# Kernel optimization log

Hardware: AMD Instinct MI355X
Metric: run time of the kernel (lower is better)

## Reference

```python
import jax, jax.numpy as jnp
import numpy as np

C = 256
GROUPS = 8
EPS_GN = 1e-5
EPS_ATTN = 1e-6


def setup_inputs() -> dict:
    key = jax.random.key(0)
    ks = jax.random.split(key, 10)
    b, c, h, w = 8, C, 128, 128
    # xavier_uniform for 1x1 conv weight [out, in]: limit = sqrt(6/(in+out))
    lim = float(np.sqrt(6.0 / (c + c)))
    mkw = lambda k: jax.random.uniform(k, (c, c), jnp.float32, -lim, lim)
    return {
        "x": jax.random.normal(ks[0], (b, c, h, w), jnp.float32),
        "gamma": jnp.ones((c,), jnp.float32),
        "beta": jnp.zeros((c,), jnp.float32),
        "Wq": mkw(ks[1]), "bq": jnp.zeros((c,), jnp.float32),
        "Wk": mkw(ks[2]), "bk": jnp.zeros((c,), jnp.float32),
        "Wv": mkw(ks[3]), "bv": jnp.zeros((c,), jnp.float32),
        "Wp": mkw(ks[4]), "bp": jnp.zeros((c,), jnp.float32),
    }


def _group_norm(x, gamma, beta):
    b, c, h, w = x.shape
    xg = x.reshape(b, GROUPS, c // GROUPS, h, w)
    mean = xg.mean(axis=(2, 3, 4), keepdims=True)
    var = xg.var(axis=(2, 3, 4), keepdims=True)
    xn = ((xg - mean) * jax.lax.rsqrt(var + EPS_GN)).reshape(b, c, h, w)
    return xn * gamma[None, :, None, None] + beta[None, :, None, None]


def _conv1x1(x, W, bias):
    # 1x1 conv == per-pixel matmul: [b,c,h,w] x [o,c] -> [b,o,h,w]
    return jnp.einsum('bchw,oc->bohw', x, W) + bias[None, :, None, None]


def reference(x, gamma, beta, Wq, bq, Wk, bk, Wv, bv, Wp, bp):
    b, c, h, w = x.shape
    xn = _group_norm(x, gamma, beta)
    q = jax.nn.elu(_conv1x1(xn, Wq, bq)) + 1.0
    k = jax.nn.elu(_conv1x1(xn, Wk, bk)) + 1.0
    v = _conv1x1(xn, Wv, bv)
    n = h * w
    q = q.reshape(b, c, n)
    k = k.reshape(b, c, n)
    v = v.reshape(b, c, n)
    kv = jnp.einsum('bcn,bdn->bcd', k, v)          # k @ v^T, [b,c,c]
    k_sum = jnp.sum(k, axis=2, keepdims=True)       # [b,c,1]
    kv = kv / (k_sum + EPS_ATTN)
    out = jnp.einsum('bcd,bdn->bcn', kv, q).reshape(b, c, h, w)
    out = _conv1x1(out, Wp, bp)
    return out + x
```

## Files before the change

### kernel.cpp

```cpp
#include <hip/hip_runtime.h>

typedef unsigned short u16;
using bf16x8 = __attribute__((ext_vector_type(8))) __bf16;
using f32x4  = __attribute__((ext_vector_type(4))) float;

#define BATCH 8
#define CH    256
#define NPIX  16384
#define GN_EPS   1e-5f
#define ATTN_EPS 1e-6f

__device__ __forceinline__ u16 f2bf(float f) {
  unsigned int u = __float_as_uint(f);
  u += 0x7fffu + ((u >> 16) & 1u);
  return (u16)(u >> 16);
}

__global__ void stats_kernel(const float* __restrict__ x, float* __restrict__ sum,
                             float* __restrict__ sqs) {
  const int gi = blockIdx.x >> 3;
  const int sp = blockIdx.x & 7;
  const float4* p = (const float4*)x + (size_t)gi * 131072 + (size_t)sp * 16384;
  float s = 0.f, ss = 0.f;
  for (int i = 0; i < 64; ++i) {
    float4 v = p[threadIdx.x + i * 256];
    s  += v.x + v.y + v.z + v.w;
    ss += v.x * v.x + v.y * v.y + v.z * v.z + v.w * v.w;
  }
  for (int off = 32; off; off >>= 1) {
    s  += __shfl_xor(s, off);
    ss += __shfl_xor(ss, off);
  }
  __shared__ float rs[4], rss[4];
  const int wave = threadIdx.x >> 6, lane = threadIdx.x & 63;
  if (!lane) { rs[wave] = s; rss[wave] = ss; }
  __syncthreads();
  if (!threadIdx.x) {
    atomicAdd(&sum[gi], rs[0] + rs[1] + rs[2] + rs[3]);
    atomicAdd(&sqs[gi], rss[0] + rss[1] + rss[2] + rss[3]);
  }
}

__global__ void finalize_kernel(const float* __restrict__ sums, const float* __restrict__ sqs,
                                const float* __restrict__ gamma, const float* __restrict__ beta,
                                float* __restrict__ sA, float* __restrict__ sB) {
  const int t = blockIdx.x * 256 + threadIdx.x;
  const int c = t & 255;
  const int gi = (t >> 8) * 8 + (c >> 5);
  const float inv = 1.f / 524288.f;
  const float mean = sums[gi] * inv;
  const float var = sqs[gi] * inv - mean * mean;
  const float rstd = rsqrtf(var + GN_EPS);
  const float a = rstd * gamma[c];
  sA[t] = a;
  sB[t] = beta[c] - mean * a;
}

__global__ __launch_bounds__(256) void foldw_kernel(
    const float* __restrict__ Wq, const float* __restrict__ bq,
    const float* __restrict__ Wk, const float* __restrict__ bk,
    const float* __restrict__ sA, const float* __restrict__ sB,
    u16* __restrict__ Wqb, u16* __restrict__ Wkb,
    float* __restrict__ bqf, float* __restrict__ bkf) {
  const int b = blockIdx.x >> 4;
  const int rt = blockIdx.x & 15;
  const int tid = threadIdx.x;
  const int wave = tid >> 6, lane = tid & 63;
  const float a = sA[b * 256 + tid];
  const float s = sB[b * 256 + tid];
  __shared__ float rq[4], rk[4];
  for (int i = 0; i < 16; ++i) {
    const int row = rt * 16 + i;
    const float wq = Wq[row * 256 + tid];
    const float wk = Wk[row * 256 + tid];
    Wqb[b * 65536 + row * 256 + tid] = f2bf(wq * a);
    Wkb[b * 65536 + row * 256 + tid] = f2bf(wk * a);
    float pq = wq * s, pk = wk * s;
    for (int off = 32; off; off >>= 1) {
      pq += __shfl_xor(pq, off);
      pk += __shfl_xor(pk, off);
    }
    if (!lane) { rq[wave] = pq; rk[wave] = pk; }
    __syncthreads();
    if (!tid) {
      bqf[b * 256 + row] = bq[row] + rq[0] + rq[1] + rq[2] + rq[3];
      bkf[b * 256 + row] = bk[row] + rk[0] + rk[1] + rk[2] + rk[3];
    }
    __syncthreads();
  }
}

__global__ __launch_bounds__(256) void wvt_kernel(const float* __restrict__ Wv,
                                                  float* __restrict__ Wvt) {
  __shared__ float t[16][17];
  const int ti = blockIdx.x & 15, tj = blockIdx.x >> 4;
  const int tx = threadIdx.x & 15, ty = threadIdx.x >> 4;
  t[ty][tx] = Wv[(tj * 16 + ty) * 256 + ti * 16 + tx];
  __syncthreads();
  Wvt[(ti * 16 + ty) * 256 + tj * 16 + tx] = t[tx][ty];
}

__global__ __launch_bounds__(1024, 4) void fused_t_kernel(
    const float* __restrict__ x, const u16* __restrict__ Wkb, const float* __restrict__ bkf,
    float* __restrict__ ksum, float* __restrict__ tdst, int mode) {
  __shared__ __align__(16) u16 xnv[64 * 288];
  __shared__ __align__(16) u16 xcm[256 * 72];
  __shared__ __align__(16) u16 Kcp[256 * 72];

  const int b  = blockIdx.x & 7;
  const int sp = blockIdx.x >> 3;
  const int tid = threadIdx.x;
  const int wave = tid >> 6;
  const int lane = tid & 63;
  const int m = lane & 15;
  const int q = lane >> 4;

  const int ctg = wave & 7;
  const int ptg = wave >> 3;
  const int ckg = wave >> 2;
  const int cvg = wave & 3;

  const float* xb = x + (size_t)b * CH * NPIX;
  const u16* Wkbb = Wkb + b * 65536;

  float biasv[2][4];
#pragma unroll
  for (int i = 0; i < 2; ++i)
#pragma unroll
    for (int r = 0; r < 4; ++r)
      biasv[i][r] = bkf[b * 256 + (2 * ctg + i) * 16 + q * 4 + r];

  f32x4 accT[4][4];
#pragma unroll
  for (int i = 0; i < 4; ++i)
#pragma unroll
    for (int j = 0; j < 4; ++j) accT[i][j] = {0.f, 0.f, 0.f, 0.f};
  float ksum_acc = 0.f;

  const int p_ = tid & 63;
  const int cq = tid >> 6;

  for (int ch = 0; ch < 8; ++ch) {
    const int pix0 = sp * 512 + ch * 64;
    __syncthreads();
#pragma unroll
    for (int i = 0; i < 4; ++i) {
      const int c = (cq + 16 * i) * 4;
      const float v0 = __builtin_nontemporal_load(&xb[(size_t)(c + 0) * NPIX + pix0 + p_]);
      const float v1 = __builtin_nontemporal_load(&xb[(size_t)(c + 1) * NPIX + pix0 + p_]);
      const float v2 = __builtin_nontemporal_load(&xb[(size_t)(c + 2) * NPIX + pix0 + p_]);
      const float v3 = __builtin_nontemporal_load(&xb[(size_t)(c + 3) * NPIX + pix0 + p_]);
      const u16 b0 = f2bf(v0), b1 = f2bf(v1), b2 = f2bf(v2), b3 = f2bf(v3);
      const unsigned int lo = (unsigned int)b0 | ((unsigned int)b1 << 16);
      const unsigned int hi = (unsigned int)b2 | ((unsigned int)b3 << 16);
      *(uint2*)&xnv[p_ * 288 + (c ^ ((p_ & 7) << 3))] = make_uint2(lo, hi);
      xcm[(c + 0) * 72 + p_] = b0;
      xcm[(c + 1) * 72 + p_] = b1;
      xcm[(c + 2) * 72 + p_] = b2;
      xcm[(c + 3) * 72 + p_] = b3;
    }
    __syncthreads();

    f32x4 ac[2][2];
#pragma unroll
    for (int i = 0; i < 2; ++i)
#pragma unroll
      for (int pp = 0; pp < 2; ++pp) ac[i][pp] = {0.f, 0.f, 0.f, 0.f};
#pragma unroll
    for (int ks = 0; ks < 8; ++ks) {
      const bf16x8 a0 = *(const bf16x8*)(Wkbb + ((2 * ctg + 0) * 16 + m) * 256 + ks * 32 + q * 8);
      const bf16x8 a1 = *(const bf16x8*)(Wkbb + ((2 * ctg + 1) * 16 + m) * 256 + ks * 32 + q * 8);
#pragma unroll
      for (int pp = 0; pp < 2; ++pp) {
        const int prow = (2 * ptg + pp) * 16 + m;
        const bf16x8 bfr =
            *(const bf16x8*)&xnv[prow * 288 + ((ks * 32 + q * 8) ^ ((prow & 7) << 3))];
        ac[0][pp] = __builtin_amdgcn_mfma_f32_16x16x32_bf16(a0, bfr, ac[0][pp], 0, 0, 0);
        ac[1][pp] = __builtin_amdgcn_mfma_f32_16x16x32_bf16(a1, bfr, ac[1][pp], 0, 0, 0);
      }
    }
#pragma unroll
    for (int i = 0; i < 2; ++i) {
#pragma unroll
      for (int r = 0; r < 4; ++r) {
        const int row = (2 * ctg + i) * 16 + q * 4 + r;
        const float bias = biasv[i][r];
#pragma unroll
        for (int pp = 0; pp < 2; ++pp) {
          float v = ac[i][pp][r] + bias;
          v = v > 0.f ? v + 1.f : __expf(v);
          Kcp[row * 72 + (2 * ptg + pp) * 16 + m] = f2bf(v);
        }
      }
    }
    __syncthreads();

    {
      const int krow = tid & 255;
      const int kseg = tid >> 8;
      const bf16x8 k0 = *(const bf16x8*)&Kcp[krow * 72 + kseg * 16];
      const bf16x8 k1 = *(const bf16x8*)&Kcp[krow * 72 + kseg * 16 + 8];
      float s = 0.f;
#pragma unroll
      for (int j = 0; j < 8; ++j) s += (float)k0[j] + (float)k1[j];
      ksum_acc += s;
    }

#pragma unroll
    for (int ks = 0; ks < 2; ++ks) {
      bf16x8 af[4], bfv[4];
#pragma unroll
      for (int i = 0; i < 4; ++i)
        af[i] = *(const bf16x8*)&Kcp[((4 * ckg + i) * 16 + m) * 72 + ks * 32 + q * 8];
#pragma unroll
      for (int j = 0; j < 4; ++j)
        bfv[j] = *(const bf16x8*)&xcm[((4 * cvg + j) * 16 + m) * 72 + ks * 32 + q * 8];
#pragma unroll
      for (int i = 0; i < 4; ++i)
#pragma unroll
        for (int j = 0; j < 4; ++j)
          accT[i][j] = __builtin_amdgcn_mfma_f32_16x16x32_bf16(af[i], bfv[j], accT[i][j], 0, 0, 0);
    }
  }

  atomicAdd(&ksum[b * CH + (tid & 255)], ksum_acc);
  if (mode == 0) {
    float* Tp = tdst + (size_t)blockIdx.x * 65536 + wave * 4096 + lane * 4;
#pragma unroll
    for (int i = 0; i < 4; ++i)
#pragma unroll
      for (int j = 0; j < 4; ++j)
        __builtin_nontemporal_store(accT[i][j], (f32x4*)(Tp + (i * 4 + j) * 256));
  } else {
    float* Tb2 = tdst + (size_t)b * 65536;
#pragma unroll
    for (int i = 0; i < 4; ++i)
#pragma unroll
      for (int j = 0; j < 4; ++j)
#pragma unroll
        for (int r = 0; r < 4; ++r) {
          const int row = (4 * ckg + i) * 16 + q * 4 + r;
          const int col = (4 * cvg + j) * 16 + m;
          atomicAdd(&Tb2[row * CH + col], accT[i][j][r]);
        }
  }
}

__global__ __launch_bounds__(256) void treduce_kernel(const float* __restrict__ part,
                                                      float* __restrict__ Traw) {
  const int b = blockIdx.x >> 4;
  const int w = blockIdx.x & 15;
  __shared__ float tile[64][65];
  const size_t base = (size_t)w * 4096;
  for (int k = 0; k < 16; ++k) {
    const int o = k * 256 + threadIdx.x;
    float s = 0.f;
#pragma unroll 8
    for (int sp = 0; sp < 32; ++sp)
      s += __builtin_nontemporal_load(&part[(size_t)(sp * 8 + b) * 65536 + base + o]);
    const int lanef = (o >> 2) & 63;
    const int r = o & 3;
    const int e4 = o >> 8;
    const int i = e4 >> 2, j = e4 & 3;
    const int mm = lanef & 15, qq = lanef >> 4;
    tile[i * 16 + qq * 4 + r][j * 16 + mm] = s;
  }
  __syncthreads();
  const int ckg = w >> 2, cvg = w & 3;
  float* dst = Traw + (size_t)b * 65536 + (size_t)(ckg * 64) * 256 + cvg * 64;
  const int col = threadIdx.x & 63;
  const int r0 = threadIdx.x >> 6;
#pragma unroll
  for (int k = 0; k < 16; ++k) {
    const int lr = r0 * 16 + k;
    dst[(size_t)lr * 256 + col] = tile[lr][col];
  }
}

__global__ __launch_bounds__(256) void m1_kernel(
    const float* __restrict__ Wp, const float* __restrict__ Traw,
    const float* __restrict__ ksum, const float* __restrict__ sA,
    const float* __restrict__ sB, float* __restrict__ A1, float* __restrict__ s1) {
  __shared__ float WpLT[256 * 16];
  __shared__ float ksL[256];
  const int b = blockIdx.x >> 4;
  const int rt = blockIdx.x & 15;
  const int tid = threadIdx.x;
  const float kk = ksum[b * 256 + tid];
  ksL[tid] = kk;
  const float rs = 1.f / (kk + ATTN_EPS);
#pragma unroll
  for (int r = 0; r < 16; ++r)
    WpLT[tid * 16 + r] = Wp[(rt * 16 + r) * 256 + tid] * rs;
  __syncthreads();
  float acc[16], s1a[16];
#pragma unroll
  for (int r = 0; r < 16; ++r) { acc[r] = 0.f; s1a[r] = 0.f; }
  const float* Tb = Traw + (size_t)b * 65536;
  for (int k = 0; k < 256; ++k) {
    const float v = Tb[k * 256 + tid];
    const float kv = ksL[k];
#pragma unroll
    for (int r4 = 0; r4 < 4; ++r4) {
      const f32x4 w4 = *(const f32x4*)&WpLT[k * 16 + r4 * 4];
#pragma unroll
      for (int e = 0; e < 4; ++e) {
        acc[r4 * 4 + e] += w4[e] * v;
        s1a[r4 * 4 + e] += w4[e] * kv;
      }
    }
  }
  const float av = sA[b * 256 + tid], sv = sB[b * 256 + tid];
#pragma unroll
  for (int r = 0; r < 16; ++r)
    A1[(size_t)b * 65536 + (rt * 16 + r) * 256 + tid] = av * acc[r] + sv * s1a[r];
  if (tid == 0) {
#pragma unroll
    for (int r = 0; r < 16; ++r) s1[b * 256 + rt * 16 + r] = s1a[r];
  }
}

__global__ __launch_bounds__(256) void m2_kernel(
    const float* __restrict__ A1, const float* __restrict__ Wvt,
    const float* __restrict__ bv, const float* __restrict__ s1,
    u16* __restrict__ Mb) {
  __shared__ float ALT[256 * 16];
  const int b = blockIdx.x >> 4;
  const int rt = blockIdx.x & 15;
  const int tid = threadIdx.x;
#pragma unroll
  for (int r = 0; r < 16; ++r)
    ALT[tid * 16 + r] = A1[(size_t)b * 65536 + (rt * 16 + r) * 256 + tid];
  __syncthreads();
  float acc[16];
#pragma unroll
  for (int r = 0; r < 16; ++r) acc[r] = 0.f;
  for (int ci = 0; ci < 256; ++ci) {
    const float wv = Wvt[ci * 256 + tid];
#pragma unroll
    for (int r4 = 0; r4 < 4; ++r4) {
      const f32x4 a4 = *(const f32x4*)&ALT[ci * 16 + r4 * 4];
#pragma unroll
      for (int e = 0; e < 4; ++e) acc[r4 * 4 + e] += a4[e] * wv;
    }
  }
  const float bvd = bv[tid];
#pragma unroll
  for (int r = 0; r < 16; ++r)
    Mb[(size_t)b * 65536 + (rt * 16 + r) * 256 + tid] =
        f2bf(acc[r] + bvd * s1[b * 256 + rt * 16 + r]);
}

__global__ __launch_bounds__(256, 4) void out_kernel(
    const float* __restrict__ x, const u16* __restrict__ Wqb, const float* __restrict__ bqf,
    const u16* __restrict__ Mb, const float* __restrict__ bp, float* __restrict__ out) {
  __shared__ __align__(16) u16 buf[64 * 288];
  const int b = blockIdx.x & 7;
  const int pix0 = (blockIdx.x >> 3) * 64;
  const int tid = threadIdx.x;
  const int wave = tid >> 6;
  const int lane = tid & 63;
  const int m = lane & 15;
  const int q = lane >> 4;

  const float* xb = x + (size_t)b * CH * NPIX;
  const u16* Wqbb = Wqb + b * 65536;

  const int p_ = tid & 63;
  const int cq = tid >> 6;
#pragma unroll
  for (int i = 0; i < 16; ++i) {
    const int c = (cq + 4 * i) * 4;
    const float v0 = __builtin_nontemporal_load(&xb[(size_t)(c + 0) * NPIX + pix0 + p_]);
    const float v1 = __builtin_nontemporal_load(&xb[(size_t)(c + 1) * NPIX + pix0 + p_]);
    const float v2 = __builtin_nontemporal_load(&xb[(size_t)(c + 2) * NPIX + pix0 + p_]);
    const float v3 = __builtin_nontemporal_load(&xb[(size_t)(c + 3) * NPIX + pix0 + p_]);
    const unsigned int lo = (unsigned int)f2bf(v0) | ((unsigned int)f2bf(v1) << 16);
    const unsigned int hi = (unsigned int)f2bf(v2) | ((unsigned int)f2bf(v3) << 16);
    *(uint2*)&buf[p_ * 288 + (c ^ ((p_ & 7) << 3))] = make_uint2(lo, hi);
  }
  __syncthreads();

  f32x4 aq[4][4];
#pragma unroll
  for (int pt = 0; pt < 4; ++pt)
#pragma unroll
    for (int ct = 0; ct < 4; ++ct) aq[pt][ct] = {0.f, 0.f, 0.f, 0.f};
#pragma unroll
  for (int ks = 0; ks < 8; ++ks) {
    bf16x8 af[4];
#pragma unroll
    for (int pt = 0; pt < 4; ++pt) {
      const int prow = pt * 16 + m;
      af[pt] = *(const bf16x8*)&buf[prow * 288 + ((ks * 32 + q * 8) ^ ((prow & 7) << 3))];
    }
#pragma unroll
    for (int ct = 0; ct < 4; ++ct) {
      const bf16x8 bfr = *(const bf16x8*)(Wqbb + ((4 * wave + ct) * 16 + m) * 256 + ks * 32 + q * 8);
#pragma unroll
      for (int pt = 0; pt < 4; ++pt)
        aq[pt][ct] = __builtin_amdgcn_mfma_f32_16x16x32_bf16(af[pt], bfr, aq[pt][ct], 0, 0, 0);
    }
  }
  __syncthreads();
#pragma unroll
  for (int ct = 0; ct < 4; ++ct) {
    const int c2 = (4 * wave + ct) * 16 + m;
    const float bias = bqf[b * 256 + c2];
#pragma unroll
    for (int pt = 0; pt < 4; ++pt)
#pragma unroll
      for (int r = 0; r < 4; ++r) {
        float v = aq[pt][ct][r] + bias;
        v = v > 0.f ? v + 1.f : __expf(v);
        const int prow = pt * 16 + q * 4 + r;
        buf[prow * 288 + (c2 ^ ((prow & 7) << 3))] = f2bf(v);
      }
  }
  __syncthreads();

  f32x4 ao[4][4];
#pragma unroll
  for (int ct = 0; ct < 4; ++ct)
#pragma unroll
    for (int pt = 0; pt < 4; ++pt) ao[ct][pt] = {0.f, 0.f, 0.f, 0.f};
  const u16* Ab = Mb + (size_t)b * 65536;
#pragma unroll
  for (int ks = 0; ks < 8; ++ks) {
    bf16x8 af2[4];
#pragma unroll
    for (int ct = 0; ct < 4; ++ct)
      af2[ct] = *(const bf16x8*)(Ab + ((4 * wave + ct) * 16 + m) * 256 + ks * 32 + q * 8);
#pragma unroll
    for (int pt = 0; pt < 4; ++pt) {
      const int brow = pt * 16 + m;
      const bf16x8 bfr = *(const bf16x8*)&buf[brow * 288 + ((ks * 32 + q * 8) ^ ((brow & 7) << 3))];
#pragma unroll
      for (int ct = 0; ct < 4; ++ct)
        ao[ct][pt] = __builtin_amdgcn_mfma_f32_16x16x32_bf16(af2[ct], bfr, ao[ct][pt], 0, 0, 0);
    }
  }
  float* ob = out + (size_t)b * CH * NPIX;
#pragma unroll
  for (int ct = 0; ct < 4; ++ct)
#pragma unroll
    for (int r = 0; r < 4; ++r) {
      const int row = (4 * wave + ct) * 16 + q * 4 + r;
      const float bias = bp[row];
#pragma unroll
      for (int pt = 0; pt < 4; ++pt) {
        const int idx = row * NPIX + pix0 + pt * 16 + m;
        const float xr = __builtin_nontemporal_load(&xb[idx]);
        __builtin_nontemporal_store(ao[ct][pt][r] + bias + xr, &ob[idx]);
      }
    }
}

extern "C" void kernel_launch(void* const* d_in, const int* in_sizes, int n_in,
                              void* d_out, int out_size, void* d_ws, size_t ws_size,
                              hipStream_t stream) {
  const float* x     = (const float*)d_in[0];
  const float* gamma = (const float*)d_in[1];
  const float* beta  = (const float*)d_in[2];
  const float* Wq    = (const float*)d_in[3];
  const float* bq    = (const float*)d_in[4];
  const float* Wk    = (const float*)d_in[5];
  const float* bk    = (const float*)d_in[6];
  const float* Wv    = (const float*)d_in[7];
  const float* bv    = (const float*)d_in[8];
  const float* Wp    = (const float*)d_in[9];
  const float* bp    = (const float*)d_in[10];
  float* out = (float*)d_out;

  float* wsf  = (float*)d_ws;
  float* sum  = wsf;
  float* sqs  = wsf + 64;
  float* ksum = wsf + 128;
  float* sA   = wsf + 2176;
  float* sB   = wsf + 4224;
  float* s1   = wsf + 6272;
  float* bkf  = wsf + 8320;
  float* bqf  = wsf + 10368;
  float* Wvt  = wsf + 12416;
  float* Traw = wsf + 77952;
  float* A1   = wsf + 602240;
  u16* Wqb = (u16*)(wsf + 1126528);
  u16* Wkb = Wqb + 524288;
  u16* Mb  = (u16*)(wsf + 1650816);

  const bool bigws = ws_size >= ((size_t)72 << 20);
  float* Tpart = bigws ? (wsf + ((size_t)1 << 21)) : Traw;
  const int mode = bigws ? 0 : 1;

  hipMemsetAsync(wsf, 0, (size_t)(bigws ? 2176 : 602240) * sizeof(float), stream);
  stats_kernel<<<512, 256, 0, stream>>>(x, sum, sqs);
  finalize_kernel<<<8, 256, 0, stream>>>(sum, sqs, gamma, beta, sA, sB);
  wvt_kernel<<<256, 256, 0, stream>>>(Wv, Wvt);
  foldw_kernel<<<128, 256, 0, stream>>>(Wq, bq, Wk, bk, sA, sB, Wqb, Wkb, bqf, bkf);
  fused_t_kernel<<<256, 1024, 0, stream>>>(x, Wkb, bkf, ksum, Tpart, mode);
  if (bigws) treduce_kernel<<<128, 256, 0, stream>>>(Tpart, Traw);
  m1_kernel<<<128, 256, 0, stream>>>(Wp, Traw, ksum, sA, sB, A1, s1);
  m2_kernel<<<128, 256, 0, stream>>>(A1, Wvt, bv, s1, Mb);
  out_kernel<<<2048, 256, 0, stream>>>(x, Wqb, bqf, Mb, bp, out);
}
```

Baseline: 680.6 us.

## Hold weight fragments in registers and make out/fused kernels persistent over pixel chunks

```diff
diff --git a/kernel.cpp b/kernel.cpp
--- a/kernel.cpp
+++ b/kernel.cpp
@@ -100,7 +100,7 @@
   Wvt[(ti * 16 + ty) * 256 + tj * 16 + tx] = t[tx][ty];
 }
 
-__global__ __launch_bounds__(1024, 4) void fused_t_kernel(
+__global__ __launch_bounds__(512, 2) void fused_t_kernel(
     const float* __restrict__ x, const u16* __restrict__ Wkb, const float* __restrict__ bkf,
     float* __restrict__ ksum, float* __restrict__ tdst, int mode) {
   __shared__ __align__(16) u16 xnv[64 * 288];
@@ -115,24 +115,29 @@
   const int m = lane & 15;
   const int q = lane >> 4;
 
-  const int ctg = wave & 7;
-  const int ptg = wave >> 3;
   const int ckg = wave >> 2;
   const int cvg = wave & 3;
 
   const float* xb = x + (size_t)b * CH * NPIX;
   const u16* Wkbb = Wkb + b * 65536;
 
+  bf16x8 wA[2][8];
+#pragma unroll
+  for (int i = 0; i < 2; ++i)
+#pragma unroll
+    for (int ks = 0; ks < 8; ++ks)
+      wA[i][ks] = *(const bf16x8*)(Wkbb + ((2 * wave + i) * 16 + m) * 256 + ks * 32 + q * 8);
+
   float biasv[2][4];
 #pragma unroll
   for (int i = 0; i < 2; ++i)
 #pragma unroll
     for (int r = 0; r < 4; ++r)
-      biasv[i][r] = bkf[b * 256 + (2 * ctg + i) * 16 + q * 4 + r];
-
-  f32x4 accT[4][4];
-#pragma unroll
-  for (int i = 0; i < 4; ++i)
+      biasv[i][r] = bkf[b * 256 + (2 * wave + i) * 16 + q * 4 + r];
+
+  f32x4 accT[8][4];
+#pragma unroll
+  for (int i = 0; i < 8; ++i)
 #pragma unroll
     for (int j = 0; j < 4; ++j) accT[i][j] = {0.f, 0.f, 0.f, 0.f};
   float ksum_acc = 0.f;
@@ -144,8 +149,8 @@
     const int pix0 = sp * 512 + ch * 64;
     __syncthreads();
 #pragma unroll
-    for (int i = 0; i < 4; ++i) {
-      const int c = (cq + 16 * i) * 4;
+    for (int i = 0; i < 8; ++i) {
+      const int c = (cq + 8 * i) * 4;
       const float v0 = __builtin_nontemporal_load(&xb[(size_t)(c + 0) * NPIX + pix0 + p_]);
       const float v1 = __builtin_nontemporal_load(&xb[(size_t)(c + 1) * NPIX + pix0 + p_]);
       const float v2 = __builtin_nontemporal_load(&xb[(size_t)(c + 2) * NPIX + pix0 + p_]);
@@ -161,35 +166,35 @@
     }
     __syncthreads();
 
-    f32x4 ac[2][2];
-#pragma unroll
-    for (int i = 0; i < 2; ++i)
-#pragma unroll
-      for (int pp = 0; pp < 2; ++pp) ac[i][pp] = {0.f, 0.f, 0.f, 0.f};
-#pragma unroll
-    for (int ks = 0; ks < 8; ++ks) {
-      const bf16x8 a0 = *(const bf16x8*)(Wkbb + ((2 * ctg + 0) * 16 + m) * 256 + ks * 32 + q * 8);
-      const bf16x8 a1 = *(const bf16x8*)(Wkbb + ((2 * ctg + 1) * 16 + m) * 256 + ks * 32 + q * 8);
-#pragma unroll
-      for (int pp = 0; pp < 2; ++pp) {
-        const int prow = (2 * ptg + pp) * 16 + m;
-        const bf16x8 bfr =
-            *(const bf16x8*)&xnv[prow * 288 + ((ks * 32 + q * 8) ^ ((prow & 7) << 3))];
-        ac[0][pp] = __builtin_amdgcn_mfma_f32_16x16x32_bf16(a0, bfr, ac[0][pp], 0, 0, 0);
-        ac[1][pp] = __builtin_amdgcn_mfma_f32_16x16x32_bf16(a1, bfr, ac[1][pp], 0, 0, 0);
-      }
-    }
-#pragma unroll
-    for (int i = 0; i < 2; ++i) {
-#pragma unroll
-      for (int r = 0; r < 4; ++r) {
-        const int row = (2 * ctg + i) * 16 + q * 4 + r;
-        const float bias = biasv[i][r];
+#pragma unroll
+    for (int ph = 0; ph < 2; ++ph) {
+      f32x4 ac[2][2];
+#pragma unroll
+      for (int i = 0; i < 2; ++i)
+#pragma unroll
+        for (int pp = 0; pp < 2; ++pp) ac[i][pp] = {0.f, 0.f, 0.f, 0.f};
+#pragma unroll
+      for (int ks = 0; ks < 8; ++ks) {
 #pragma unroll
         for (int pp = 0; pp < 2; ++pp) {
-          float v = ac[i][pp][r] + bias;
-          v = v > 0.f ? v + 1.f : __expf(v);
-          Kcp[row * 72 + (2 * ptg + pp) * 16 + m] = f2bf(v);
+          const int prow = (2 * ph + pp) * 16 + m;
+          const bf16x8 bfr =
+              *(const bf16x8*)&xnv[prow * 288 + ((ks * 32 + q * 8) ^ ((prow & 7) << 3))];
+          ac[0][pp] = __builtin_amdgcn_mfma_f32_16x16x32_bf16(wA[0][ks], bfr, ac[0][pp], 0, 0, 0);
+          ac[1][pp] = __builtin_amdgcn_mfma_f32_16x16x32_bf16(wA[1][ks], bfr, ac[1][pp], 0, 0, 0);
+        }
+      }
+#pragma unroll
+      for (int i = 0; i < 2; ++i) {
+#pragma unroll
+        for (int r = 0; r < 4; ++r) {
+          const int row = (2 * wave + i) * 16 + q * 4 + r;
+#pragma unroll
+          for (int pp = 0; pp < 2; ++pp) {
+            float v = ac[i][pp][r] + biasv[i][r];
+            v = v > 0.f ? v + 1.f : __expf(v);
+            Kcp[row * 72 + (2 * ph + pp) * 16 + m] = f2bf(v);
+          }
         }
       }
     }
@@ -198,49 +203,50 @@
     {
       const int krow = tid & 255;
       const int kseg = tid >> 8;
-      const bf16x8 k0 = *(const bf16x8*)&Kcp[krow * 72 + kseg * 16];
-      const bf16x8 k1 = *(const bf16x8*)&Kcp[krow * 72 + kseg * 16 + 8];
       float s = 0.f;
 #pragma unroll
-      for (int j = 0; j < 8; ++j) s += (float)k0[j] + (float)k1[j];
+      for (int t2 = 0; t2 < 4; ++t2) {
+        const bf16x8 k0 = *(const bf16x8*)&Kcp[krow * 72 + kseg * 32 + t2 * 8];
+#pragma unroll
+        for (int j = 0; j < 8; ++j) s += (float)k0[j];
+      }
       ksum_acc += s;
     }
 
 #pragma unroll
     for (int ks = 0; ks < 2; ++ks) {
-      bf16x8 af[4], bfv[4];
-#pragma unroll
-      for (int i = 0; i < 4; ++i)
-        af[i] = *(const bf16x8*)&Kcp[((4 * ckg + i) * 16 + m) * 72 + ks * 32 + q * 8];
+      bf16x8 bfv[4];
 #pragma unroll
       for (int j = 0; j < 4; ++j)
         bfv[j] = *(const bf16x8*)&xcm[((4 * cvg + j) * 16 + m) * 72 + ks * 32 + q * 8];
 #pragma unroll
-      for (int i = 0; i < 4; ++i)
+      for (int i = 0; i < 8; ++i) {
+        const bf16x8 afi = *(const bf16x8*)&Kcp[((8 * ckg + i) * 16 + m) * 72 + ks * 32 + q * 8];
 #pragma unroll
         for (int j = 0; j < 4; ++j)
-          accT[i][j] = __builtin_amdgcn_mfma_f32_16x16x32_bf16(af[i], bfv[j], accT[i][j], 0, 0, 0);
+          accT[i][j] = __builtin_amdgcn_mfma_f32_16x16x32_bf16(afi, bfv[j], accT[i][j], 0, 0, 0);
+      }
     }
   }
 
   atomicAdd(&ksum[b * CH + (tid & 255)], ksum_acc);
   if (mode == 0) {
-    float* Tp = tdst + (size_t)blockIdx.x * 65536 + wave * 4096 + lane * 4;
-#pragma unroll
-    for (int i = 0; i < 4; ++i)
+    float* Tp = tdst + (size_t)blockIdx.x * 65536 + wave * 8192 + lane * 4;
+#pragma unroll
+    for (int i = 0; i < 8; ++i)
 #pragma unroll
       for (int j = 0; j < 4; ++j)
-        __builtin_nontemporal_store(accT[i][j], (f32x4*)(Tp + (i * 4 + j) * 256));
+        *(f32x4*)(Tp + (i * 4 + j) * 256) = accT[i][j];
   } else {
     float* Tb2 = tdst + (size_t)b * 65536;
 #pragma unroll
-    for (int i = 0; i < 4; ++i)
+    for (int i = 0; i < 8; ++i)
 #pragma unroll
       for (int j = 0; j < 4; ++j)
 #pragma unroll
         for (int r = 0; r < 4; ++r) {
-          const int row = (4 * ckg + i) * 16 + q * 4 + r;
-          const int col = (4 * cvg + j) * 16 + m;
+          const int row = ckg * 128 + i * 16 + q * 4 + r;
+          const int col = cvg * 64 + j * 16 + m;
           atomicAdd(&Tb2[row * CH + col], accT[i][j][r]);
         }
   }
@@ -248,32 +254,35 @@
 
 __global__ __launch_bounds__(256) void treduce_kernel(const float* __restrict__ part,
                                                       float* __restrict__ Traw) {
-  const int b = blockIdx.x >> 4;
-  const int w = blockIdx.x & 15;
-  __shared__ float tile[64][65];
-  const size_t base = (size_t)w * 4096;
-  for (int k = 0; k < 16; ++k) {
-    const int o = k * 256 + threadIdx.x;
-    float s = 0.f;
+  const int b = blockIdx.x >> 5;
+  const int w = (blockIdx.x >> 2) & 7;
+  const int s = blockIdx.x & 3;
+  const int tid = threadIdx.x;
+  __shared__ float tile[32][65];
+  const int base = w * 8192 + s * 2048;
+  for (int k = 0; k < 8; ++k) {
+    const int f = base + k * 256 + tid;
+    float acc = 0.f;
 #pragma unroll 8
-    for (int sp = 0; sp < 32; ++sp)
-      s += __builtin_nontemporal_load(&part[(size_t)(sp * 8 + b) * 65536 + base + o]);
-    const int lanef = (o >> 2) & 63;
-    const int r = o & 3;
-    const int e4 = o >> 8;
-    const int i = e4 >> 2, j = e4 & 3;
+    for (int spp = 0; spp < 32; ++spp)
+      acc += part[(size_t)(spp * 8 + b) * 65536 + f];
+    const int il = k >> 2;
+    const int j = k & 3;
+    const int lanef = tid >> 2;
+    const int r = tid & 3;
     const int mm = lanef & 15, qq = lanef >> 4;
-    tile[i * 16 + qq * 4 + r][j * 16 + mm] = s;
+    tile[il * 16 + qq * 4 + r][j * 16 + mm] = acc;
   }
   __syncthreads();
-  const int ckg = w >> 2, cvg = w & 3;
-  float* dst = Traw + (size_t)b * 65536 + (size_t)(ckg * 64) * 256 + cvg * 64;
-  const int col = threadIdx.x & 63;
-  const int r0 = threadIdx.x >> 6;
-#pragma unroll
-  for (int k = 0; k < 16; ++k) {
-    const int lr = r0 * 16 + k;
-    dst[(size_t)lr * 256 + col] = tile[lr][col];
+  const int rowbase = (w >> 2) * 128 + s * 32;
+  const int colbase = (w & 3) * 64;
+  const int cl = tid & 63;
+  const int rl0 = tid >> 6;
+  float* dst = Traw + (size_t)b * 65536;
+#pragma unroll
+  for (int k = 0; k < 8; ++k) {
+    const int rl = rl0 * 8 + k;
+    dst[(size_t)(rowbase + rl) * 256 + colbase + cl] = tile[rl][cl];
   }
 }
 
@@ -351,12 +360,12 @@
         f2bf(acc[r] + bvd * s1[b * 256 + rt * 16 + r]);
 }
 
-__global__ __launch_bounds__(256, 4) void out_kernel(
+__global__ __launch_bounds__(512, 2) void out_kernel(
     const float* __restrict__ x, const u16* __restrict__ Wqb, const float* __restrict__ bqf,
     const u16* __restrict__ Mb, const float* __restrict__ bp, float* __restrict__ out) {
   __shared__ __align__(16) u16 buf[64 * 288];
   const int b = blockIdx.x & 7;
-  const int pix0 = (blockIdx.x >> 3) * 64;
+  const int sp = blockIdx.x >> 3;
   const int tid = threadIdx.x;
   const int wave = tid >> 6;
   const int lane = tid & 63;
@@ -365,95 +374,107 @@
 
   const float* xb = x + (size_t)b * CH * NPIX;
   const u16* Wqbb = Wqb + b * 65536;
+  const u16* Ab = Mb + (size_t)b * 65536;
+
+  bf16x8 wQ[2][8], wM[2][8];
+#pragma unroll
+  for (int ct = 0; ct < 2; ++ct)
+#pragma unroll
+    for (int ks = 0; ks < 8; ++ks) {
+      wQ[ct][ks] = *(const bf16x8*)(Wqbb + ((2 * wave + ct) * 16 + m) * 256 + ks * 32 + q * 8);
+      wM[ct][ks] = *(const bf16x8*)(Ab + ((2 * wave + ct) * 16 + m) * 256 + ks * 32 + q * 8);
+    }
+  float biasq[2], biasp[2][4];
+#pragma unroll
+  for (int ct = 0; ct < 2; ++ct) {
+    biasq[ct] = bqf[b * 256 + (2 * wave + ct) * 16 + m];
+#pragma unroll
+    for (int r = 0; r < 4; ++r) biasp[ct][r] = bp[(2 * wave + ct) * 16 + q * 4 + r];
+  }
 
   const int p_ = tid & 63;
   const int cq = tid >> 6;
-#pragma unroll
-  for (int i = 0; i < 16; ++i) {
-    const int c = (cq + 4 * i) * 4;
-    const float v0 = __builtin_nontemporal_load(&xb[(size_t)(c + 0) * NPIX + pix0 + p_]);
-    const float v1 = __builtin_nontemporal_load(&xb[(size_t)(c + 1) * NPIX + pix0 + p_]);
-    const float v2 = __builtin_nontemporal_load(&xb[(size_t)(c + 2) * NPIX + pix0 + p_]);
-    const float v3 = __builtin_nontemporal_load(&xb[(size_t)(c + 3) * NPIX + pix0 + p_]);
-    const unsigned int lo = (unsigned int)f2bf(v0) | ((unsigned int)f2bf(v1) << 16);
-    const unsigned int hi = (unsigned int)f2bf(v2) | ((unsigned int)f2bf(v3) << 16);
-    *(uint2*)&buf[p_ * 288 + (c ^ ((p_ & 7) << 3))] = make_uint2(lo, hi);
-  }
-  __syncthreads();
-
-  f32x4 aq[4][4];
-#pragma unroll
-  for (int pt = 0; pt < 4; ++pt)
-#pragma unroll
-    for (int ct = 0; ct < 4; ++ct) aq[pt][ct] = {0.f, 0.f, 0.f, 0.f};
-#pragma unroll
-  for (int ks = 0; ks < 8; ++ks) {
-    bf16x8 af[4];
-#pragma unroll
-    for (int pt = 0; pt < 4; ++pt) {
-      const int prow = pt * 16 + m;
-      af[pt] = *(const bf16x8*)&buf[prow * 288 + ((ks * 32 + q * 8) ^ ((prow & 7) << 3))];
-    }
-#pragma unroll
-    for (int ct = 0; ct < 4; ++ct) {
-      const bf16x8 bfr = *(const bf16x8*)(Wqbb + ((4 * wave + ct) * 16 + m) * 256 + ks * 32 + q * 8);
+
+  for (int ch = 0; ch < 8; ++ch) {
+    const int pix0 = sp * 512 + ch * 64;
+    __syncthreads();
+#pragma unroll
+    for (int i = 0; i < 8; ++i) {
+      const int c = (cq + 8 * i) * 4;
+      const float v0 = __builtin_nontemporal_load(&xb[(size_t)(c + 0) * NPIX + pix0 + p_]);
+      const float v1 = __builtin_nontemporal_load(&xb[(size_t)(c + 1) * NPIX + pix0 + p_]);
+      const float v2 = __builtin_nontemporal_load(&xb[(size_t)(c + 2) * NPIX + pix0 + p_]);
+      const float v3 = __builtin_nontemporal_load(&xb[(size_t)(c + 3) * NPIX + pix0 + p_]);
+      const unsigned int lo = (unsigned int)f2bf(v0) | ((unsigned int)f2bf(v1) << 16);
+      const unsigned int hi = (unsigned int)f2bf(v2) | ((unsigned int)f2bf(v3) << 16);
+      *(uint2*)&buf[p_ * 288 + (c ^ ((p_ & 7) << 3))] = make_uint2(lo, hi);
+    }
+    __syncthreads();
+
+    f32x4 aq[4][2];
+#pragma unroll
+    for (int pt = 0; pt < 4; ++pt)
+#pragma unroll
+      for (int ct = 0; ct < 2; ++ct) aq[pt][ct] = {0.f, 0.f, 0.f, 0.f};
+#pragma unroll
+    for (int ks = 0; ks < 8; ++ks) {
+#pragma unroll
+      for (int pt = 0; pt < 4; ++pt) {
+        const int prow = pt * 16 + m;
+        const bf16x8 af =
+            *(const bf16x8*)&buf[prow * 288 + ((ks * 32 + q * 8) ^ ((prow & 7) << 3))];
+#pragma unroll
+        for (int ct = 0; ct < 2; ++ct)
+          aq[pt][ct] = __builtin_amdgcn_mfma_f32_16x16x32_bf16(af, wQ[ct][ks], aq[pt][ct], 0, 0, 0);
+      }
+    }
+    __syncthreads();
+#pragma unroll
+    for (int ct = 0; ct < 2; ++ct) {
+      const int c2 = (2 * wave + ct) * 16 + m;
 #pragma unroll
       for (int pt = 0; pt < 4; ++pt)
-        aq[pt][ct] = __builtin_amdgcn_mfma_f32_16x16x32_bf16(af[pt], bfr, aq[pt][ct], 0, 0, 0);
-    }
-  }
-  __syncthreads();
-#pragma unroll
-  for (int ct = 0; ct < 4; ++ct) {
-    const int c2 = (4 * wave + ct) * 16 + m;
-    const float bias = bqf[b * 256 + c2];
-#pragma unroll
-    for (int pt = 0; pt < 4; ++pt)
+#pragma unroll
+        for (int r = 0; r < 4; ++r) {
+          float v = aq[pt][ct][r] + biasq[ct];
+          v = v > 0.f ? v + 1.f : __expf(v);
+          const int prow = pt * 16 + q * 4 + r;
+          buf[prow * 288 + (c2 ^ ((prow & 7) << 3))] = f2bf(v);
+        }
+    }
+    __syncthreads();
+
+    f32x4 ao[2][4];
+#pragma unroll
+    for (int ct = 0; ct < 2; ++ct)
+#pragma unroll
+      for (int pt = 0; pt < 4; ++pt) ao[ct][pt] = {0.f, 0.f, 0.f, 0.f};
+#pragma unroll
+    for (int ks = 0; ks < 8; ++ks) {
+#pragma unroll
+      for (int pt = 0; pt < 4; ++pt) {
+        const int brow = pt * 16 + m;
+        const bf16x8 bfr =
+            *(const bf16x8*)&buf[brow * 288 + ((ks * 32 + q * 8) ^ ((brow & 7) << 3))];
+#pragma unroll
+        for (int ct = 0; ct < 2; ++ct)
+          ao[ct][pt] = __builtin_amdgcn_mfma_f32_16x16x32_bf16(wM[ct][ks], bfr, ao[ct][pt], 0, 0, 0);
+      }
+    }
+    float* ob = out + (size_t)b * CH * NPIX;
+#pragma unroll
+    for (int ct = 0; ct < 2; ++ct)
 #pragma unroll
       for (int r = 0; r < 4; ++r) {
-        float v = aq[pt][ct][r] + bias;
-        v = v > 0.f ? v + 1.f : __expf(v);
-        const int prow = pt * 16 + q * 4 + r;
-        buf[prow * 288 + (c2 ^ ((prow & 7) << 3))] = f2bf(v);
-      }
-  }
-  __syncthreads();
-
-  f32x4 ao[4][4];
-#pragma unroll
-  for (int ct = 0; ct < 4; ++ct)
-#pragma unroll
-    for (int pt = 0; pt < 4; ++pt) ao[ct][pt] = {0.f, 0.f, 0.f, 0.f};
-  const u16* Ab = Mb + (size_t)b * 65536;
-#pragma unroll
-  for (int ks = 0; ks < 8; ++ks) {
-    bf16x8 af2[4];
-#pragma unroll
-    for (int ct = 0; ct < 4; ++ct)
-      af2[ct] = *(const bf16x8*)(Ab + ((4 * wave + ct) * 16 + m) * 256 + ks * 32 + q * 8);
-#pragma unroll
-    for (int pt = 0; pt < 4; ++pt) {
-      const int brow = pt * 16 + m;
-      const bf16x8 bfr = *(const bf16x8*)&buf[brow * 288 + ((ks * 32 + q * 8) ^ ((brow & 7) << 3))];
-#pragma unroll
-      for (int ct = 0; ct < 4; ++ct)
-        ao[ct][pt] = __builtin_amdgcn_mfma_f32_16x16x32_bf16(af2[ct], bfr, ao[ct][pt], 0, 0, 0);
-    }
-  }
-  float* ob = out + (size_t)b * CH * NPIX;
-#pragma unroll
-  for (int ct = 0; ct < 4; ++ct)
-#pragma unroll
-    for (int r = 0; r < 4; ++r) {
-      const int row = (4 * wave + ct) * 16 + q * 4 + r;
-      const float bias = bp[row];
-#pragma unroll
-      for (int pt = 0; pt < 4; ++pt) {
-        const int idx = row * NPIX + pix0 + pt * 16 + m;
-        const float xr = __builtin_nontemporal_load(&xb[idx]);
-        __builtin_nontemporal_store(ao[ct][pt][r] + bias + xr, &ob[idx]);
-      }
-    }
+        const int row = (2 * wave + ct) * 16 + q * 4 + r;
+#pragma unroll
+        for (int pt = 0; pt < 4; ++pt) {
+          const int idx = row * NPIX + pix0 + pt * 16 + m;
+          const float xr = __builtin_nontemporal_load(&xb[idx]);
+          __builtin_nontemporal_store(ao[ct][pt][r] + biasp[ct][r] + xr, &ob[idx]);
+        }
+      }
+  }
 }
 
 extern "C" void kernel_launch(void* const* d_in, const int* in_sizes, int n_in,
@@ -497,9 +518,9 @@
   finalize_kernel<<<8, 256, 0, stream>>>(sum, sqs, gamma, beta, sA, sB);
   wvt_kernel<<<256, 256, 0, stream>>>(Wv, Wvt);
   foldw_kernel<<<128, 256, 0, stream>>>(Wq, bq, Wk, bk, sA, sB, Wqb, Wkb, bqf, bkf);
-  fused_t_kernel<<<256, 1024, 0, stream>>>(x, Wkb, bkf, ksum, Tpart, mode);
-  if (bigws) treduce_kernel<<<128, 256, 0, stream>>>(Tpart, Traw);
+  fused_t_kernel<<<256, 512, 0, stream>>>(x, Wkb, bkf, ksum, Tpart, mode);
+  if (bigws) treduce_kernel<<<256, 256, 0, stream>>>(Tpart, Traw);
   m1_kernel<<<128, 256, 0, stream>>>(Wp, Traw, ksum, sA, sB, A1, s1);
   m2_kernel<<<128, 256, 0, stream>>>(A1, Wvt, bv, s1, Mb);
-  out_kernel<<<2048, 256, 0, stream>>>(x, Wqb, bqf, Mb, bp, out);
-}
+  out_kernel<<<256, 512, 0, stream>>>(x, Wqb, bqf, Mb, bp, out);
+}
```

Result: slower. 873.9 us (+28.4%).
